# Kernel optimization log

Measured on AMD Instinct MI355X. Metric: run time of the kernel, lower is better.

Reference implementation:

```python
import jax, jax.numpy as jnp
import numpy as np


def conv1x1(x, w, b):
    # x: [B,Cin,H,W], w: [Cout,Cin], b: [Cout]
    return jnp.einsum('bchw,oc->bohw', x, w) + b[None, :, None, None]


def _lin_idx_w(in_size, out_size):
    # PyTorch bilinear, align_corners=False: src = max((i+0.5)*scale - 0.5, 0)
    scale = in_size / out_size
    src = jnp.maximum((jnp.arange(out_size, dtype=jnp.float32) + 0.5) * scale - 0.5, 0.0)
    i0 = jnp.floor(src).astype(jnp.int32)
    i0 = jnp.minimum(i0, in_size - 1)
    i1 = jnp.minimum(i0 + 1, in_size - 1)
    w1 = src - i0.astype(jnp.float32)
    return i0, i1, w1


def bilinear_resize(x, out_h, out_w):
    Hin, Win = x.shape[-2], x.shape[-1]
    y0, y1, wy = _lin_idx_w(Hin, out_h)
    x0, x1, wx = _lin_idx_w(Win, out_w)
    wy = wy[:, None]  # [out_h,1]
    rows = x[:, :, y0, :] * (1.0 - wy) + x[:, :, y1, :] * wy
    out = rows[:, :, :, x0] * (1.0 - wx) + rows[:, :, :, x1] * wx      # [B,C,out_h,out_w]
    return out


def setup_inputs() -> dict:
    key = jax.random.key(0)
    ks = jax.random.split(key, 10)
    C, C8 = 512, 64
    s = 1.0 / np.sqrt(C)
    return {
        'content': jax.random.normal(ks[0], (4, C, 64, 64), jnp.float32),
        'style': jax.random.normal(ks[1], (4, C, 80, 80), jnp.float32),
        'f_w': jax.random.normal(ks[2], (C8, C), jnp.float32) * s,
        'f_b': jax.random.normal(ks[3], (C8,), jnp.float32) * 0.01,
        'g_w': jax.random.normal(ks[4], (C8, C), jnp.float32) * s,
        'g_b': jax.random.normal(ks[5], (C8,), jnp.float32) * 0.01,
        'h_w': jax.random.normal(ks[6], (C, C), jnp.float32) * s,
        'h_b': jax.random.normal(ks[7], (C,), jnp.float32) * 0.01,
        'out_w': jax.random.normal(ks[8], (C, C), jnp.float32) * s,
        'out_b': jax.random.normal(ks[9], (C,), jnp.float32) * 0.01,
    }


def reference(content, style, f_w, f_b, g_w, g_b, h_w, h_b, out_w, out_b):
    B, C, H, W = content.shape
    HW = H * W
    f = conv1x1(content, f_w, f_b).reshape(B, -1, HW)                       # [B,C8,HW] (query, pre-transpose)
    g = bilinear_resize(conv1x1(style, g_w, g_b), H, W).reshape(B, -1, HW)  # [B,C8,HW]
    h = bilinear_resize(conv1x1(style, h_w, h_b), H, W).reshape(B, C, HW)   # [B,C,HW]
    attn = jax.nn.softmax(jnp.einsum('bcm,bcn->bmn', f, g), axis=-1)        # [B,HW_q,HW_k]
    out = jnp.einsum('bcn,bmn->bcm', h, attn).reshape(B, C, H, W)
    return conv1x1(out, out_w, out_b)
```

## Files before the change

kernel.cpp:

```cpp
#include <hip/hip_runtime.h>

#define NB 4
#define NC 512
#define ND 64
#define HW 4096
#define SPIN 6400

typedef _Float16 f16;
typedef _Float16 f16x8 __attribute__((ext_vector_type(8)));
typedef short s16x8 __attribute__((ext_vector_type(8)));
typedef float f32x4 __attribute__((ext_vector_type(4)));

__device__ __forceinline__ unsigned short f32_to_bf16(float x) {
  union { float f; unsigned u; } v; v.f = x;
  unsigned r = v.u + 0x7FFFu + ((v.u >> 16) & 1u);
  return (unsigned short)(r >> 16);
}

__device__ __forceinline__ void stv(float* p, float v) { *p = v; }
__device__ __forceinline__ void stv(f16* p, float v) { *p = (f16)v; }
__device__ __forceinline__ void stv(unsigned short* p, float v) { *p = f32_to_bf16(v); }

__global__ __launch_bounds__(256) void cvtw_kernel(const float* __restrict__ fw,
                                                   const float* __restrict__ gw,
                                                   const float* __restrict__ hw,
                                                   const float* __restrict__ ow,
                                                   f16* __restrict__ dst) {
  int i = blockIdx.x * 256 + threadIdx.x;
  const float* src; int off;
  if (i < 32768) { src = fw; off = 0; }
  else if (i < 65536) { src = gw; off = 32768; }
  else if (i < 327680) { src = hw; off = 65536; }
  else { src = ow; off = 327680; }
  dst[i] = (f16)src[i - off];
}

__global__ __launch_bounds__(256) void tcvt_kernel(const float* __restrict__ in,
                                                   f16* __restrict__ out) {
  __shared__ float Xs[64][65];
  int p0 = blockIdx.x * 64, c0 = blockIdx.y * 64, b = blockIdx.z;
  int t = threadIdx.x;
  const float* ib = in + ((size_t)b * NC + c0) * HW + p0;
  int pl = t & 63, cg = t >> 6;
#pragma unroll
  for (int k = 0; k < 16; ++k) {
    int c = cg * 16 + k;
    Xs[c][pl] = ib[(size_t)c * HW + pl];
  }
  __syncthreads();
  int p = t >> 2, cb = (t & 3) * 16;
  union { f16 h[16]; float4 q[2]; } u;
#pragma unroll
  for (int j = 0; j < 16; ++j) u.h[j] = (f16)Xs[cb + j][p];
  f16* ob = out + ((size_t)b * HW + p0 + p) * NC + c0 + cb;
  *(float4*)(ob) = u.q[0];
  *(float4*)(ob + 8) = u.q[1];
}

__global__ __launch_bounds__(256) void rstcvt_kernel(const float* __restrict__ X,
                                                     f16* __restrict__ Y) {
  __shared__ float Xs[64 * 165];
  int oy = blockIdx.x, c0 = blockIdx.y * 64, b = blockIdx.z;
  float syf = fmaxf((oy + 0.5f) * 1.25f - 0.5f, 0.f);
  int y0 = (int)syf; int y1 = min(y0 + 1, 79); float wy = syf - (float)y0;
  int t = threadIdx.x;
  const float* Xb = X + ((size_t)b * NC + c0) * SPIN;
#pragma unroll
  for (int k = 0; k < 10; ++k) {
    int idx = t + k * 256;
    int c = idx / 40;
    int rem = idx - c * 40;
    int yy = rem / 20;
    int x4 = rem - yy * 20;
    int ysrc = yy ? y1 : y0;
    float4 v = *(const float4*)(Xb + (size_t)c * SPIN + ysrc * 80 + x4 * 4);
    float* d = Xs + c * 165 + yy * 82 + x4 * 4;
    d[0] = v.x; d[1] = v.y; d[2] = v.z; d[3] = v.w;
  }
  __syncthreads();
  int ox = t >> 2, cb = (t & 3) * 16;
  float sxf = fmaxf((ox + 0.5f) * 1.25f - 0.5f, 0.f);
  int x0 = (int)sxf; int x1 = min(x0 + 1, 79); float wx = sxf - (float)x0;
  union { f16 h[16]; float4 q[2]; } u;
#pragma unroll
  for (int j = 0; j < 16; ++j) {
    const float* base = Xs + (cb + j) * 165;
    float a0 = base[x0], a1 = base[x1];
    float b0 = base[82 + x0], b1 = base[82 + x1];
    float r0 = a0 + (a1 - a0) * wx;
    float r1 = b0 + (b1 - b0) * wx;
    u.h[j] = (f16)(r0 + (r1 - r0) * wy);
  }
  f16* ob = Y + ((size_t)b * HW + oy * 64 + ox) * NC + c0 + cb;
  *(float4*)(ob) = u.q[0];
  *(float4*)(ob + 8) = u.q[1];
}

__global__ __launch_bounds__(256) void convpm2_kernel(const f16* __restrict__ X0,
                                                      const f16* __restrict__ X1,
                                                      const f16* __restrict__ W01,
                                                      const float* __restrict__ b0,
                                                      const float* __restrict__ b1,
                                                      f16* __restrict__ Y0,
                                                      f16* __restrict__ Y1) {
  int sel = blockIdx.z >> 2;
  int b = blockIdx.z & 3;
  const f16* X = sel ? X1 : X0;
  const f16* W = W01 + sel * (ND * NC);
  const float* bias = sel ? b1 : b0;
  f16* Y = sel ? Y1 : Y0;
  int t = threadIdx.x, l = t & 63, w = t >> 6;
  int pw = blockIdx.x * 256 + w * 64;
  int l4 = l & 15, g = l >> 4;
  f32x4 acc[4][4] = {};
  const f16* Xb = X + ((size_t)b * HW + pw) * NC;
  for (int kk = 0; kk < 16; ++kk) {
    int co = kk * 32 + g * 8;
    f16x8 a[4], bb[4];
#pragma unroll
    for (int ms = 0; ms < 4; ++ms) a[ms] = *(const f16x8*)(Xb + (size_t)(ms * 16 + l4) * NC + co);
#pragma unroll
    for (int ct = 0; ct < 4; ++ct) bb[ct] = *(const f16x8*)(W + (size_t)(ct * 16 + l4) * NC + co);
#pragma unroll
    for (int ms = 0; ms < 4; ++ms)
#pragma unroll
      for (int ct = 0; ct < 4; ++ct)
        acc[ms][ct] = __builtin_amdgcn_mfma_f32_16x16x32_f16(a[ms], bb[ct], acc[ms][ct], 0, 0, 0);
  }
  float bv[4];
#pragma unroll
  for (int ct = 0; ct < 4; ++ct) bv[ct] = bias[ct * 16 + l4];
  f16* Yb = Y + ((size_t)b * HW + pw) * ND;
#pragma unroll
  for (int ms = 0; ms < 4; ++ms)
#pragma unroll
    for (int ct = 0; ct < 4; ++ct)
#pragma unroll
      for (int r = 0; r < 4; ++r)
        Yb[(size_t)(ms * 16 + g * 4 + r) * ND + ct * 16 + l4] = (f16)(acc[ms][ct][r] + bv[ct]);
}

template <typename OUT_T>
__global__ __launch_bounds__(256) void convcm_kernel(const f16* __restrict__ X,
                                                     const f16* __restrict__ W,
                                                     const float* __restrict__ bias,
                                                     OUT_T* __restrict__ Y, int O) {
  int b = blockIdx.z;
  int o0 = blockIdx.x * 64;
  int t = threadIdx.x, l = t & 63, w = t >> 6;
  int pw = blockIdx.y * 256 + w * 64;
  int l4 = l & 15, g = l >> 4;
  f32x4 acc[4][4] = {};
  const f16* Xb = X + ((size_t)b * HW + pw) * NC;
  const f16* Wb = W + (size_t)o0 * NC;
  for (int kk = 0; kk < 16; ++kk) {
    int co = kk * 32 + g * 8;
    f16x8 a[4], bb[4];
#pragma unroll
    for (int ms = 0; ms < 4; ++ms) a[ms] = *(const f16x8*)(Wb + (size_t)(ms * 16 + l4) * NC + co);
#pragma unroll
    for (int ct = 0; ct < 4; ++ct) bb[ct] = *(const f16x8*)(Xb + (size_t)(ct * 16 + l4) * NC + co);
#pragma unroll
    for (int ms = 0; ms < 4; ++ms)
#pragma unroll
      for (int ct = 0; ct < 4; ++ct)
        acc[ms][ct] = __builtin_amdgcn_mfma_f32_16x16x32_f16(a[ms], bb[ct], acc[ms][ct], 0, 0, 0);
  }
  float bv[4][4];
#pragma unroll
  for (int ms = 0; ms < 4; ++ms)
#pragma unroll
    for (int r = 0; r < 4; ++r) bv[ms][r] = bias[o0 + ms * 16 + g * 4 + r];
#pragma unroll
  for (int ms = 0; ms < 4; ++ms)
#pragma unroll
    for (int ct = 0; ct < 4; ++ct)
#pragma unroll
      for (int r = 0; r < 4; ++r) {
        float val = acc[ms][ct][r] + bv[ms][r];
        stv(&Y[((size_t)b * O + o0 + ms * 16 + g * 4 + r) * HW + pw + ct * 16 + l4], val);
      }
}

__global__ __launch_bounds__(512, 4) void attn_kernel(const f16* __restrict__ FT,
                                                      const f16* __restrict__ GT,
                                                      const unsigned short* __restrict__ HC,
                                                      f16* __restrict__ MIDT) {
  __shared__ __align__(16) char KsB[2][128 * 128];
  __shared__ __align__(16) char PsB[64 * 256];
  __shared__ float denP[8][16];
  int bid = blockIdx.x;
  int b = (bid & 7) >> 1;
  int cs = bid & 1;
  int m0 = (bid >> 3) * 64;
  int t = threadIdx.x, l = t & 63, w = t >> 6;
  int l4 = l & 15, g = l >> 4;
  int msq = w >> 1;
  int nsq = (w & 1) * 4;

  const f16* Fb = FT + ((size_t)b * HW + m0 + msq * 16 + l4) * ND + g * 8;
  f16x8 qa0 = *(const f16x8*)(Fb);
  f16x8 qa1 = *(const f16x8*)(Fb + 32);

  f32x4 acc[4][2] = {};
  float den_acc[4] = {0.f, 0.f, 0.f, 0.f};

  const f16* Gb = GT + (size_t)b * HW * ND;
  const unsigned short* Hb = HC + ((size_t)b * NC + cs * 256 + w * 32) * HW;

  int nl0 = t >> 3, cc0 = t & 7;
  int ka0 = (nl0 * 128 + cc0 * 16) ^ ((nl0 & 7) << 4);
  const f16* gsrc0 = Gb + (size_t)nl0 * ND + cc0 * 8;

  const unsigned short* hb0 = Hb + (size_t)l4 * HW + g * 8;
  const unsigned short* hb1 = Hb + (size_t)(16 + l4) * HW + g * 8;

  {
    f16x8 k0 = *(const f16x8*)(gsrc0);
    f16x8 k1 = *(const f16x8*)(gsrc0 + (size_t)64 * ND);
    *(f16x8*)(KsB[0] + ka0) = k0;
    *(f16x8*)(KsB[0] + ka0 + 8192) = k1;
  }
  __syncthreads();

  int cur = 0;
  for (int it = 0; it < 32; ++it) {
    int n0 = it * 128;
    bool pre = (it < 31);
    f16x8 k0, k1;
    if (pre) {
      const f16* gs = gsrc0 + (size_t)(n0 + 128) * ND;
      k0 = *(const f16x8*)(gs);
      k1 = *(const f16x8*)(gs + (size_t)64 * ND);
    }
    s16x8 vb00 = *(const s16x8*)(hb0 + n0);
    s16x8 vb01 = *(const s16x8*)(hb0 + n0 + 32);
    s16x8 vb10 = *(const s16x8*)(hb1 + n0);
    s16x8 vb11 = *(const s16x8*)(hb1 + n0 + 32);

    const char* Kc = KsB[cur];
#pragma unroll
    for (int f = 0; f < 4; ++f) {
      int n = (nsq + f) * 16 + l4;
      int sw = (n & 7) << 4;
      f16x8 kb0 = *(const f16x8*)(Kc + ((n * 128 + g * 16) ^ sw));
      f16x8 kb1 = *(const f16x8*)(Kc + ((n * 128 + 64 + g * 16) ^ sw));
      f32x4 s = {};
      s = __builtin_amdgcn_mfma_f32_16x16x32_f16(qa0, kb0, s, 0, 0, 0);
      s = __builtin_amdgcn_mfma_f32_16x16x32_f16(qa1, kb1, s, 0, 0, 0);
#pragma unroll
      for (int r = 0; r < 4; ++r) {
        float p = __expf(s[r]);
        den_acc[r] += p;
        int row = msq * 16 + g * 4 + r;
        *(unsigned short*)(PsB + ((row * 256 + n * 2) ^ ((row & 7) << 4))) = f32_to_bf16(p);
      }
    }
    __syncthreads();
    if (pre) {
      *(f16x8*)(KsB[cur ^ 1] + ka0) = k0;
      *(f16x8*)(KsB[cur ^ 1] + ka0 + 8192) = k1;
    }
    s16x8 wb00 = *(const s16x8*)(hb0 + n0 + 64);
    s16x8 wb01 = *(const s16x8*)(hb0 + n0 + 96);
    s16x8 wb10 = *(const s16x8*)(hb1 + n0 + 64);
    s16x8 wb11 = *(const s16x8*)(hb1 + n0 + 96);
#pragma unroll
    for (int khh = 0; khh < 2; ++khh) {
      s16x8 v00 = khh ? wb00 : vb00, v01 = khh ? wb01 : vb01;
      s16x8 v10 = khh ? wb10 : vb10, v11 = khh ? wb11 : vb11;
#pragma unroll
      for (int mh = 0; mh < 2; ++mh) {
        s16x8 pa[2][2];
#pragma unroll
        for (int mi = 0; mi < 2; ++mi) {
          int row = (mh * 2 + mi) * 16 + l4;
          int sw = (row & 7) << 4;
          pa[mi][0] = *(const s16x8*)(PsB + ((row * 256 + khh * 128 + g * 16) ^ sw));
          pa[mi][1] = *(const s16x8*)(PsB + ((row * 256 + khh * 128 + 64 + g * 16) ^ sw));
        }
        __builtin_amdgcn_s_setprio(1);
#pragma unroll
        for (int mi = 0; mi < 2; ++mi) {
          int ms = mh * 2 + mi;
          acc[ms][0] = __builtin_amdgcn_mfma_f32_16x16x32_bf16(pa[mi][0], v00, acc[ms][0], 0, 0, 0);
          acc[ms][0] = __builtin_amdgcn_mfma_f32_16x16x32_bf16(pa[mi][1], v01, acc[ms][0], 0, 0, 0);
          acc[ms][1] = __builtin_amdgcn_mfma_f32_16x16x32_bf16(pa[mi][0], v10, acc[ms][1], 0, 0, 0);
          acc[ms][1] = __builtin_amdgcn_mfma_f32_16x16x32_bf16(pa[mi][1], v11, acc[ms][1], 0, 0, 0);
        }
        __builtin_amdgcn_s_setprio(0);
      }
    }
    __syncthreads();
    cur ^= 1;
  }

#pragma unroll
  for (int r = 0; r < 4; ++r) {
    float v = den_acc[r];
    v += __shfl_xor(v, 1); v += __shfl_xor(v, 2);
    v += __shfl_xor(v, 4); v += __shfl_xor(v, 8);
    den_acc[r] = v;
  }
  if (l4 == 0) {
#pragma unroll
    for (int r = 0; r < 4; ++r) denP[w][g * 4 + r] = den_acc[r];
  }
  __syncthreads();
  f16* Mb = MIDT + ((size_t)b * HW + m0) * NC + cs * 256 + w * 32;
#pragma unroll
  for (int ms = 0; ms < 4; ++ms)
#pragma unroll
    for (int r = 0; r < 4; ++r) {
      float rd = 1.f / (denP[2 * ms][g * 4 + r] + denP[2 * ms + 1][g * 4 + r]);
#pragma unroll
      for (int ct = 0; ct < 2; ++ct)
        Mb[(size_t)(ms * 16 + g * 4 + r) * NC + ct * 16 + l4] = (f16)(acc[ms][ct][r] * rd);
    }
}

extern "C" void kernel_launch(void* const* d_in, const int* in_sizes, int n_in,
                              void* d_out, int out_size, void* d_ws, size_t ws_size,
                              hipStream_t stream) {
  const float* content = (const float*)d_in[0];
  const float* style   = (const float*)d_in[1];
  const float* f_w = (const float*)d_in[2];
  const float* f_b = (const float*)d_in[3];
  const float* g_w = (const float*)d_in[4];
  const float* g_b = (const float*)d_in[5];
  const float* h_w = (const float*)d_in[6];
  const float* h_b = (const float*)d_in[7];
  const float* out_w = (const float*)d_in[8];
  const float* out_b = (const float*)d_in[9];
  float* out = (float*)d_out;

  const size_t MB = 1ull << 20;
  char* base = (char*)d_ws;
  f16* contentT = (f16*)base;
  f16* midT     = (f16*)base;
  unsigned short* hC = (unsigned short*)(base + 16 * MB);
  f16* fT = (f16*)(base + 32 * MB);
  f16* gT = (f16*)(base + 34 * MB);
  f16* styrT = (f16*)(base + 48 * MB);
  f16* w16 = (f16*)(base + 64 * MB);
  f16* fw16 = w16;
  f16* gw16 = w16 + 32768;
  f16* hw16 = w16 + 65536;
  f16* ow16 = w16 + 327680;

  cvtw_kernel<<<dim3(589824 / 256), 256, 0, stream>>>(f_w, g_w, h_w, out_w, w16);
  tcvt_kernel<<<dim3(HW / 64, NC / 64, NB), 256, 0, stream>>>(content, contentT);
  rstcvt_kernel<<<dim3(64, NC / 64, NB), 256, 0, stream>>>(style, styrT);
  convpm2_kernel<<<dim3(HW / 256, 1, 2 * NB), 256, 0, stream>>>(contentT, styrT, fw16, f_b, g_b, fT, gT);
  convcm_kernel<unsigned short><<<dim3(NC / 64, HW / 256, NB), 256, 0, stream>>>(styrT, hw16, h_b, hC, NC);
  attn_kernel<<<dim3(512), 512, 0, stream>>>(fT, gT, hC, midT);
  convcm_kernel<float><<<dim3(NC / 64, HW / 256, NB), 256, 0, stream>>>(midT, ow16, out_b, out, NC);
}
```

Measured before the change: 291.7 us.

## Restructure attention kernel so each wave owns its P tile and skips the mid-iteration barrier

The attention kernel is re-tiled so each block covers 32 query rows and all 512 channels. Each wave computes its own 16 rows by 128 keys of scores with the Q/K operand order swapped, so it writes and reads a private P tile with only a waitcnt and no block barrier. The exp values are packed into bf16 pairs with the HIP intrinsic and stored as 64-bit writes. The softmax denominator is reduced with two shuffles. The price is that every wave recomputes the full QK^T for its rows, four times the score work per block. The PV step also now streams 8 channel fragments of V straight from global memory with software prefetch, which raises register pressure and global traffic per wave.

```diff
diff --git a/kernel.cpp b/kernel.cpp
--- a/kernel.cpp
+++ b/kernel.cpp
@@ -1,4 +1,5 @@
 #include <hip/hip_runtime.h>
+#include <hip/hip_bf16.h>
 
 #define NB 4
 #define NC 512
@@ -10,6 +11,7 @@
 typedef _Float16 f16x8 __attribute__((ext_vector_type(8)));
 typedef short s16x8 __attribute__((ext_vector_type(8)));
 typedef float f32x4 __attribute__((ext_vector_type(4)));
+typedef unsigned short ushortT;
 
 __device__ __forceinline__ unsigned short f32_to_bf16(float x) {
   union { float f; unsigned u; } v; v.f = x;
@@ -20,6 +22,12 @@
 __device__ __forceinline__ void stv(float* p, float v) { *p = v; }
 __device__ __forceinline__ void stv(f16* p, float v) { *p = (f16)v; }
 __device__ __forceinline__ void stv(unsigned short* p, float v) { *p = f32_to_bf16(v); }
+
+__device__ __forceinline__ unsigned pk_bf16(float a, float b) {
+  __hip_bfloat162 h = __float22bfloat162_rn(float2{a, b});
+  union { __hip_bfloat162 h2; unsigned u; } c; c.h2 = h;
+  return c.u;
+}
 
 __global__ __launch_bounds__(256) void cvtw_kernel(const float* __restrict__ fw,
                                                    const float* __restrict__ gw,
@@ -186,137 +194,113 @@
                                                       const f16* __restrict__ GT,
                                                       const unsigned short* __restrict__ HC,
                                                       f16* __restrict__ MIDT) {
-  __shared__ __align__(16) char KsB[2][128 * 128];
-  __shared__ __align__(16) char PsB[64 * 256];
-  __shared__ float denP[8][16];
+  __shared__ __align__(16) char LDS[65536];
   int bid = blockIdx.x;
   int b = (bid & 7) >> 1;
-  int cs = bid & 1;
-  int m0 = (bid >> 3) * 64;
+  int mt = ((bid >> 3) << 1) | (bid & 1);
+  int m0 = mt * 32;
   int t = threadIdx.x, l = t & 63, w = t >> 6;
-  int l4 = l & 15, g = l >> 4;
-  int msq = w >> 1;
-  int nsq = (w & 1) * 4;
-
-  const f16* Fb = FT + ((size_t)b * HW + m0 + msq * 16 + l4) * ND + g * 8;
+  int l4 = l & 15, hi = l >> 4;
+  int mf = w >> 2;
+  int cq = w & 3;
+  int mr = m0 + mf * 16;
+
+  const f16* Fb = FT + ((size_t)b * HW + mr + l4) * ND + hi * 8;
   f16x8 qa0 = *(const f16x8*)(Fb);
   f16x8 qa1 = *(const f16x8*)(Fb + 32);
 
-  f32x4 acc[4][2] = {};
-  float den_acc[4] = {0.f, 0.f, 0.f, 0.f};
-
   const f16* Gb = GT + (size_t)b * HW * ND;
-  const unsigned short* Hb = HC + ((size_t)b * NC + cs * 256 + w * 32) * HW;
-
-  int nl0 = t >> 3, cc0 = t & 7;
-  int ka0 = (nl0 * 128 + cc0 * 16) ^ ((nl0 & 7) << 4);
-  const f16* gsrc0 = Gb + (size_t)nl0 * ND + cc0 * 8;
-
-  const unsigned short* hb0 = Hb + (size_t)l4 * HW + g * 8;
-  const unsigned short* hb1 = Hb + (size_t)(16 + l4) * HW + g * 8;
+  const unsigned short* Hb = HC + ((size_t)b * NC + cq * 128) * HW;
+
+  char* Ps = LDS + 32768 + w * 4096;
+  const int psw = (l4 & 7) << 4;
+
+  f32x4 acc[8] = {};
+  float den = 0.f;
+
+  int row0 = t >> 3, chunk0 = t & 7;
+  int ka0 = (row0 * 128 + chunk0 * 16) ^ ((row0 & 7) << 4);
+  int ka1 = ka0 + 64 * 128;
+  const f16* gs0 = Gb + (size_t)row0 * ND + chunk0 * 8;
+  const f16* gs1 = gs0 + (size_t)64 * ND;
 
   {
-    f16x8 k0 = *(const f16x8*)(gsrc0);
-    f16x8 k1 = *(const f16x8*)(gsrc0 + (size_t)64 * ND);
-    *(f16x8*)(KsB[0] + ka0) = k0;
-    *(f16x8*)(KsB[0] + ka0 + 8192) = k1;
+    f16x8 a = *(const f16x8*)gs0;
+    f16x8 c = *(const f16x8*)gs1;
+    *(f16x8*)(LDS + ka0) = a;
+    *(f16x8*)(LDS + ka1) = c;
   }
   __syncthreads();
 
   int cur = 0;
   for (int it = 0; it < 32; ++it) {
     int n0 = it * 128;
-    bool pre = (it < 31);
-    f16x8 k0, k1;
-    if (pre) {
-      const f16* gs = gsrc0 + (size_t)(n0 + 128) * ND;
-      k0 = *(const f16x8*)(gs);
-      k1 = *(const f16x8*)(gs + (size_t)64 * ND);
+    f16x8 kn0, kn1;
+    if (it < 31) {
+      kn0 = *(const f16x8*)(gs0 + (size_t)(n0 + 128) * ND);
+      kn1 = *(const f16x8*)(gs1 + (size_t)(n0 + 128) * ND);
     }
-    s16x8 vb00 = *(const s16x8*)(hb0 + n0);
-    s16x8 vb01 = *(const s16x8*)(hb0 + n0 + 32);
-    s16x8 vb10 = *(const s16x8*)(hb1 + n0);
-    s16x8 vb11 = *(const s16x8*)(hb1 + n0 + 32);
-
-    const char* Kc = KsB[cur];
-#pragma unroll
-    for (int f = 0; f < 4; ++f) {
-      int n = (nsq + f) * 16 + l4;
-      int sw = (n & 7) << 4;
-      f16x8 kb0 = *(const f16x8*)(Kc + ((n * 128 + g * 16) ^ sw));
-      f16x8 kb1 = *(const f16x8*)(Kc + ((n * 128 + 64 + g * 16) ^ sw));
+    const char* Kc = LDS + cur * 16384;
+#pragma unroll
+    for (int nf = 0; nf < 8; ++nf) {
+      const char* kr = Kc + (nf * 16 + l4) * 128;
+      f16x8 kb0 = *(const f16x8*)(kr + ((hi * 16) ^ psw));
+      f16x8 kb1 = *(const f16x8*)(kr + (((4 + hi) * 16) ^ psw));
       f32x4 s = {};
-      s = __builtin_amdgcn_mfma_f32_16x16x32_f16(qa0, kb0, s, 0, 0, 0);
-      s = __builtin_amdgcn_mfma_f32_16x16x32_f16(qa1, kb1, s, 0, 0, 0);
-#pragma unroll
-      for (int r = 0; r < 4; ++r) {
-        float p = __expf(s[r]);
-        den_acc[r] += p;
-        int row = msq * 16 + g * 4 + r;
-        *(unsigned short*)(PsB + ((row * 256 + n * 2) ^ ((row & 7) << 4))) = f32_to_bf16(p);
+      s = __builtin_amdgcn_mfma_f32_16x16x32_f16(kb0, qa0, s, 0, 0, 0);
+      s = __builtin_amdgcn_mfma_f32_16x16x32_f16(kb1, qa1, s, 0, 0, 0);
+      float p0 = __expf(s[0]), p1 = __expf(s[1]), p2 = __expf(s[2]), p3 = __expf(s[3]);
+      den += (p0 + p1) + (p2 + p3);
+      unsigned long long q = (unsigned long long)pk_bf16(p0, p1) |
+                             ((unsigned long long)pk_bf16(p2, p3) << 32);
+      *(unsigned long long*)(Ps + ((l4 * 256 + nf * 32 + hi * 8) ^ psw)) = q;
+    }
+    asm volatile("s_waitcnt lgkmcnt(0)" ::: "memory");
+    s16x8 pa[4];
+#pragma unroll
+    for (int kc = 0; kc < 4; ++kc)
+      pa[kc] = *(const s16x8*)(Ps + ((l4 * 256 + kc * 64 + hi * 16) ^ psw));
+    const unsigned short* hp = Hb + (size_t)l4 * HW + n0 + hi * 8;
+    s16x8 vb[4];
+#pragma unroll
+    for (int kc = 0; kc < 4; ++kc) vb[kc] = *(const s16x8*)(hp + kc * 32);
+#pragma unroll
+    for (int cf = 0; cf < 8; ++cf) {
+      s16x8 vn[4];
+      if (cf < 7) {
+        const unsigned short* hq = hp + (size_t)(cf + 1) * 16 * HW;
+#pragma unroll
+        for (int kc = 0; kc < 4; ++kc) vn[kc] = *(const s16x8*)(hq + kc * 32);
       }
+      __builtin_amdgcn_s_setprio(1);
+#pragma unroll
+      for (int kc = 0; kc < 4; ++kc)
+        acc[cf] = __builtin_amdgcn_mfma_f32_16x16x32_bf16(pa[kc], vb[kc], acc[cf], 0, 0, 0);
+      __builtin_amdgcn_s_setprio(0);
+#pragma unroll
+      for (int kc = 0; kc < 4; ++kc) vb[kc] = vn[kc];
     }
-    __syncthreads();
-    if (pre) {
-      *(f16x8*)(KsB[cur ^ 1] + ka0) = k0;
-      *(f16x8*)(KsB[cur ^ 1] + ka0 + 8192) = k1;
-    }
-    s16x8 wb00 = *(const s16x8*)(hb0 + n0 + 64);
-    s16x8 wb01 = *(const s16x8*)(hb0 + n0 + 96);
-    s16x8 wb10 = *(const s16x8*)(hb1 + n0 + 64);
-    s16x8 wb11 = *(const s16x8*)(hb1 + n0 + 96);
-#pragma unroll
-    for (int khh = 0; khh < 2; ++khh) {
-      s16x8 v00 = khh ? wb00 : vb00, v01 = khh ? wb01 : vb01;
-      s16x8 v10 = khh ? wb10 : vb10, v11 = khh ? wb11 : vb11;
-#pragma unroll
-      for (int mh = 0; mh < 2; ++mh) {
-        s16x8 pa[2][2];
-#pragma unroll
-        for (int mi = 0; mi < 2; ++mi) {
-          int row = (mh * 2 + mi) * 16 + l4;
-          int sw = (row & 7) << 4;
-          pa[mi][0] = *(const s16x8*)(PsB + ((row * 256 + khh * 128 + g * 16) ^ sw));
-          pa[mi][1] = *(const s16x8*)(PsB + ((row * 256 + khh * 128 + 64 + g * 16) ^ sw));
-        }
-        __builtin_amdgcn_s_setprio(1);
-#pragma unroll
-        for (int mi = 0; mi < 2; ++mi) {
-          int ms = mh * 2 + mi;
-          acc[ms][0] = __builtin_amdgcn_mfma_f32_16x16x32_bf16(pa[mi][0], v00, acc[ms][0], 0, 0, 0);
-          acc[ms][0] = __builtin_amdgcn_mfma_f32_16x16x32_bf16(pa[mi][1], v01, acc[ms][0], 0, 0, 0);
-          acc[ms][1] = __builtin_amdgcn_mfma_f32_16x16x32_bf16(pa[mi][0], v10, acc[ms][1], 0, 0, 0);
-          acc[ms][1] = __builtin_amdgcn_mfma_f32_16x16x32_bf16(pa[mi][1], v11, acc[ms][1], 0, 0, 0);
-        }
-        __builtin_amdgcn_s_setprio(0);
-      }
+    if (it < 31) {
+      char* Kn = LDS + (cur ^ 1) * 16384;
+      *(f16x8*)(Kn + ka0) = kn0;
+      *(f16x8*)(Kn + ka1) = kn1;
     }
     __syncthreads();
     cur ^= 1;
   }
 
-#pragma unroll
-  for (int r = 0; r < 4; ++r) {
-    float v = den_acc[r];
-    v += __shfl_xor(v, 1); v += __shfl_xor(v, 2);
-    v += __shfl_xor(v, 4); v += __shfl_xor(v, 8);
-    den_acc[r] = v;
-  }
-  if (l4 == 0) {
-#pragma unroll
-    for (int r = 0; r < 4; ++r) denP[w][g * 4 + r] = den_acc[r];
-  }
-  __syncthreads();
-  f16* Mb = MIDT + ((size_t)b * HW + m0) * NC + cs * 256 + w * 32;
-#pragma unroll
-  for (int ms = 0; ms < 4; ++ms)
-#pragma unroll
-    for (int r = 0; r < 4; ++r) {
-      float rd = 1.f / (denP[2 * ms][g * 4 + r] + denP[2 * ms + 1][g * 4 + r]);
-#pragma unroll
-      for (int ct = 0; ct < 2; ++ct)
-        Mb[(size_t)(ms * 16 + g * 4 + r) * NC + ct * 16 + l4] = (f16)(acc[ms][ct][r] * rd);
-    }
+  den += __shfl_xor(den, 16);
+  den += __shfl_xor(den, 32);
+  float rd = 1.f / den;
+  float rdv[4];
+#pragma unroll
+  for (int r = 0; r < 4; ++r) rdv[r] = __shfl(rd, hi * 4 + r);
+  f16* Mb = MIDT + ((size_t)b * HW + mr) * NC + cq * 128;
+#pragma unroll
+  for (int cf = 0; cf < 8; ++cf)
+#pragma unroll
+    for (int r = 0; r < 4; ++r)
+      Mb[(size_t)(hi * 4 + r) * NC + cf * 16 + l4] = (f16)(acc[cf][r] * rdv[r]);
 }
 
 extern "C" void kernel_launch(void* const* d_in, const int* in_sizes, int n_in,
```

Measured after the change: 607.5 us. 2.08x slower.
